# Kernel tuning notes

Measured on AMD Instinct MI355X. Metric: run time of the kernel, lower is better.

## Reference

```python
import jax, jax.numpy as jnp
import numpy as np

B, T, C, H = 2, 2048, 1024, 16
D = C // H  # head_dim = 64

def setup_inputs() -> dict:
    key = jax.random.key(0)
    k1, k2, k3 = jax.random.split(key, 3)
    x = jax.random.normal(k1, (B, T, C), dtype=jnp.float32)
    W_qkv = jax.random.normal(k2, (C, 3 * C), dtype=jnp.float32) * (C ** -0.5)
    b_qkv = jnp.zeros((3 * C,), dtype=jnp.float32)
    W_proj = jax.random.normal(k3, (C, C), dtype=jnp.float32) * (C ** -0.5)
    b_proj = jnp.zeros((C,), dtype=jnp.float32)
    return {"x": x, "W_qkv": W_qkv, "b_qkv": b_qkv, "W_proj": W_proj, "b_proj": b_proj}

def reference(x, W_qkv, b_qkv, W_proj, b_proj):
    # qkv projection: [B,T,3C]
    qkv = jnp.einsum('btc,cf->btf', x, W_qkv) + b_qkv
    q, k, v = jnp.split(qkv, 3, axis=-1)
    # split heads -> [B,H,T,D]
    q = q.reshape(B, T, H, D).transpose(0, 2, 1, 3)
    k = k.reshape(B, T, H, D).transpose(0, 2, 1, 3)
    v = v.reshape(B, T, H, D).transpose(0, 2, 1, 3)
    scale = 1.0 / jnp.sqrt(jnp.float32(D))
    att = jnp.einsum('bhqd,bhkd->bhqk', q, k) * scale  # [B,H,T,T]
    causal = jnp.tril(jnp.ones((T, T), dtype=bool))
    att = jnp.where(causal[None, None, :, :], att, jnp.float32(-jnp.inf))
    att = jax.nn.softmax(att, axis=-1)
    y = jnp.einsum('bhqk,bhkd->bhqd', att, v)  # [B,H,T,D]
    y = y.transpose(0, 2, 1, 3).reshape(B, T, C)
    return jnp.einsum('btc,cf->btf', y, W_proj) + b_proj
```

## Files before the change

### kernel.cpp

```cpp
#include <hip/hip_runtime.h>
#include <hip/hip_bf16.h>

#define Bq 2
#define Tq 2048
#define Cq 1024
#define Hq 16
#define Dq 64
#define Mq (Bq * Tq)

typedef __bf16 bf16x8 __attribute__((ext_vector_type(8)));
typedef float f32x4 __attribute__((ext_vector_type(4)));
typedef unsigned short u16;

static __device__ __forceinline__ u16 f2bf(float f) {
  union { float f; unsigned u; } v; v.f = f;
  return (u16)((v.u + 0x7fffu + ((v.u >> 16) & 1u)) >> 16);
}

static __device__ __forceinline__ f32x4 mfma16(bf16x8 a, bf16x8 b, f32x4 c) {
  return __builtin_amdgcn_mfma_f32_16x16x32_bf16(a, b, c, 0, 0, 0);
}

#define GLD16(g, l)                                                   \
  __builtin_amdgcn_global_load_lds(                                   \
      (const __attribute__((address_space(1))) unsigned int*)(g),     \
      (__attribute__((address_space(3))) unsigned int*)(l), 16, 0, 0)

static __device__ __forceinline__ int swz(int col, int row) {
  return (col & 7) + 8 * (((col >> 3) ^ (row >> 3)) & 7);
}

__global__ __launch_bounds__(256) void convert_x(const float* __restrict__ x,
                                                 u16* __restrict__ xb) {
  int i = (blockIdx.x * 256 + threadIdx.x) * 8;
  float4 a = *(const float4*)(x + i);
  float4 b = *(const float4*)(x + i + 4);
  u16 tmp[8];
  tmp[0] = f2bf(a.x); tmp[1] = f2bf(a.y); tmp[2] = f2bf(a.z); tmp[3] = f2bf(a.w);
  tmp[4] = f2bf(b.x); tmp[5] = f2bf(b.y); tmp[6] = f2bf(b.z); tmp[7] = f2bf(b.w);
  *(uint4*)(xb + i) = *(const uint4*)tmp;
}

__global__ __launch_bounds__(256) void transpose_w(const float* __restrict__ W,
                                                   u16* __restrict__ Wt,
                                                   int K, int N) {
  __shared__ __align__(16) u16 Ts[64][72];
  const int k0 = blockIdx.x * 64, n0 = blockIdx.y * 64;
  const int t = threadIdx.x;
  const int r = t >> 2, c0 = (t & 3) * 16;
  const float* src = W + (size_t)(k0 + r) * N + n0 + c0;
  u16 v16[16];
#pragma unroll
  for (int i = 0; i < 4; i++) {
    float4 f = *(const float4*)(src + 4 * i);
    v16[4 * i + 0] = f2bf(f.x); v16[4 * i + 1] = f2bf(f.y);
    v16[4 * i + 2] = f2bf(f.z); v16[4 * i + 3] = f2bf(f.w);
  }
#pragma unroll
  for (int j = 0; j < 16; j++) Ts[c0 + j][r] = v16[j];
  __syncthreads();
  u16* dst = Wt + (size_t)(n0 + r) * K + k0 + c0;
  *(uint4*)dst = *(const uint4*)&Ts[r][c0];
  *(uint4*)(dst + 8) = *(const uint4*)&Ts[r][c0 + 8];
}

__global__ __launch_bounds__(256) void qkv_gemm(
    const u16* __restrict__ A, const u16* __restrict__ Bt,
    const float* __restrict__ bias,
    u16* __restrict__ qw, u16* __restrict__ kw, u16* __restrict__ vw) {
  const int K = 1024;
  __shared__ __align__(16) u16 As[128][32];
  __shared__ __align__(16) u16 Bs[128][32];
  const int m0 = blockIdx.x * 128, n0 = blockIdx.y * 128;
  const int t = threadIdx.x, lane = t & 63, w = t >> 6;
  const int wm = (w >> 1) * 64, wn = (w & 1) * 64;
  const int l15 = lane & 15, l4 = lane >> 4;
  const int lr = lane >> 2, lc = (lane & 3) * 8;
  f32x4 acc[4][4] = {};
  const u16* ga = A + (size_t)(m0 + w * 16 + lr) * K + lc;
  const u16* gb = Bt + (size_t)(n0 + w * 16 + lr) * K + lc;

  for (int kk = 0; kk < K; kk += 32) {
    __syncthreads();
    GLD16(ga + kk, &As[w * 16][0]);
    GLD16(ga + (size_t)64 * K + kk, &As[64 + w * 16][0]);
    GLD16(gb + kk, &Bs[w * 16][0]);
    GLD16(gb + (size_t)64 * K + kk, &Bs[64 + w * 16][0]);
    __syncthreads();
    bf16x8 af[4], bfr[4];
#pragma unroll
    for (int i = 0; i < 4; i++) {
      af[i] = *(const bf16x8*)&As[wm + i * 16 + l15][l4 * 8];
      bfr[i] = *(const bf16x8*)&Bs[wn + i * 16 + l15][l4 * 8];
    }
#pragma unroll
    for (int mi = 0; mi < 4; mi++)
#pragma unroll
      for (int ni = 0; ni < 4; ni++)
        acc[mi][ni] = mfma16(af[mi], bfr[ni], acc[mi][ni]);
  }
#pragma unroll
  for (int mi = 0; mi < 4; mi++) {
#pragma unroll
    for (int ni = 0; ni < 4; ni++) {
#pragma unroll
      for (int r = 0; r < 4; r++) {
        int row = m0 + wm + mi * 16 + l4 * 4 + r;
        int col = n0 + wn + ni * 16 + l15;
        float val = acc[mi][ni][r] + bias[col];
        int which = col >> 10, c = col & 1023;
        if (which == 0) val *= 0.18033688011112042f;
        int h = c >> 6, d = c & 63;
        int b = row >> 11, tt = row & 2047;
        u16* dst = (which == 0) ? qw : ((which == 1) ? kw : vw);
        dst[(size_t)((b * Hq + h) * Tq + tt) * Dq + d] = f2bf(val);
      }
    }
  }
}

__global__ __launch_bounds__(512, 4) void attn(
    const u16* __restrict__ qw, const u16* __restrict__ kw,
    const u16* __restrict__ vw, u16* __restrict__ yw) {
  const int bh = blockIdx.x;
  const int qy = blockIdx.y;
  const int qb = (qy < 8) ? (15 - qy) : (qy - 8);
  __shared__ __align__(16) u16 Ks[64][72];
  __shared__ __align__(16) u16 Vt[64][72];
  const int t = threadIdx.x, lane = t & 63, w = t >> 6;
  const int l15 = lane & 15, l4 = lane >> 4;
  const size_t base = (size_t)bh * Tq * Dq;
  const int rv = t >> 3, c8 = t & 7;

  const int qs = qb * 128 + w * 16;
  bf16x8 qf[2];
  {
    const u16* qp = qw + base + (size_t)(qs + l15) * Dq + l4 * 8;
    qf[0] = *(const bf16x8*)qp;
    qf[1] = *(const bf16x8*)(qp + 32);
  }

  float m = -1e30f, lsum = 0.f;
  f32x4 accO[4] = {};
  const int kvmax = 2 * qb + 1;

  const u16* ksrc = kw + base + (size_t)rv * Dq + c8 * 8;
  const u16* vsrc = vw + base + (size_t)rv * Dq + c8 * 8;
  uint4 kreg = *(const uint4*)ksrc;
  uint4 vreg = *(const uint4*)vsrc;

  for (int kv = 0; kv <= kvmax; kv++) {
    __syncthreads();
    *(uint4*)&Ks[rv][c8 * 8] = kreg;
    {
      union { uint4 q; u16 s[8]; } vu; vu.q = vreg;
#pragma unroll
      for (int jj = 0; jj < 8; jj++) {
        int row = c8 * 8 + jj;
        Vt[row][swz(rv, row)] = vu.s[jj];
      }
    }
    if (kv < kvmax) {
      ksrc += 64 * Dq; vsrc += 64 * Dq;
      kreg = *(const uint4*)ksrc;
      vreg = *(const uint4*)vsrc;
    }
    __syncthreads();

    if (kv * 64 > qs + 15) continue;

    f32x4 sc[4];
    __builtin_amdgcn_s_setprio(1);
#pragma unroll
    for (int ct = 0; ct < 4; ct++) {
      bf16x8 kf0 = *(const bf16x8*)&Ks[ct * 16 + l15][l4 * 8];
      bf16x8 kf1 = *(const bf16x8*)&Ks[ct * 16 + l15][32 + l4 * 8];
      f32x4 z = {};
      z = mfma16(kf0, qf[0], z);
      z = mfma16(kf1, qf[1], z);
      sc[ct] = z;
    }
    __builtin_amdgcn_s_setprio(0);

    if (kv * 64 + 63 > qs) {
      const int q = qs + l15;
#pragma unroll
      for (int ct = 0; ct < 4; ct++)
#pragma unroll
        for (int r = 0; r < 4; r++) {
          int k = kv * 64 + ct * 16 + l4 * 4 + r;
          if (k > q) sc[ct][r] = -1e30f;
        }
    }

    float pmax = sc[0][0];
#pragma unroll
    for (int ct = 0; ct < 4; ct++)
#pragma unroll
      for (int r = 0; r < 4; r++) pmax = fmaxf(pmax, sc[ct][r]);
    pmax = fmaxf(pmax, __shfl_xor(pmax, 16));
    pmax = fmaxf(pmax, __shfl_xor(pmax, 32));

    if (__any(pmax > m + 8.f)) {
      float mn = fmaxf(m, pmax);
      float corr = exp2f(m - mn);
      m = mn;
      lsum *= corr;
#pragma unroll
      for (int r = 0; r < 4; r++) {
        float cb = __shfl(corr, (lane >> 4) * 20 + r);
#pragma unroll
        for (int dt = 0; dt < 4; dt++) accO[dt][r] *= cb;
      }
    }

    float psum = 0.f;
#pragma unroll
    for (int ct = 0; ct < 4; ct++)
#pragma unroll
      for (int r = 0; r < 4; r++) {
        float p = exp2f(sc[ct][r] - m);
        sc[ct][r] = p;
        psum += p;
      }
    psum += __shfl_xor(psum, 16);
    psum += __shfl_xor(psum, 32);
    lsum += psum;

    bf16x8 pa[2];
    const int bsrc = ((lane & 16) << 1) + l15;
#pragma unroll
    for (int h = 0; h < 2; h++) {
#pragma unroll
      for (int jh = 0; jh < 2; jh++)
#pragma unroll
        for (int r = 0; r < 4; r++) {
          float v0 = __shfl(sc[2 * h][r], bsrc + 16 * jh);
          float v1 = __shfl(sc[2 * h + 1][r], bsrc + 16 * jh);
          pa[h][jh * 4 + r] = (__bf16)((l4 & 2) ? v1 : v0);
        }
    }

    __builtin_amdgcn_s_setprio(1);
#pragma unroll
    for (int dt = 0; dt < 4; dt++) {
      int Rv = dt * 16 + l15;
      int e = (Rv >> 3) & 7;
      bf16x8 vf0 = *(const bf16x8*)&Vt[Rv][8 * ((l4 ^ e) & 7)];
      bf16x8 vf1 = *(const bf16x8*)&Vt[Rv][8 * (((4 + l4) ^ e) & 7)];
      accO[dt] = mfma16(pa[0], vf0, accO[dt]);
      accO[dt] = mfma16(pa[1], vf1, accO[dt]);
    }
    __builtin_amdgcn_s_setprio(0);
  }

  float inv = 1.0f / lsum;
  const int b = bh >> 4, hd = bh & 15;
#pragma unroll
  for (int r = 0; r < 4; r++) {
    float ib = __shfl(inv, (lane >> 4) * 20 + r);
    int tt = qs + l4 * 4 + r;
    size_t rowbase = ((size_t)(b * Tq + tt)) * Cq + hd * 64;
#pragma unroll
    for (int dt = 0; dt < 4; dt++)
      yw[rowbase + dt * 16 + l15] = f2bf(accO[dt][r] * ib);
  }
}

__global__ __launch_bounds__(256) void proj_gemm(
    const u16* __restrict__ A, const u16* __restrict__ Bt,
    const float* __restrict__ bias, float* __restrict__ out) {
  const int K = 1024, N = 1024;
  __shared__ __align__(16) u16 As[128][32];
  __shared__ __align__(16) u16 Bs[128][32];
  const int m0 = blockIdx.x * 128, n0 = blockIdx.y * 128;
  const int t = threadIdx.x, lane = t & 63, w = t >> 6;
  const int wm = (w >> 1) * 64, wn = (w & 1) * 64;
  const int l15 = lane & 15, l4 = lane >> 4;
  const int lr = lane >> 2, lc = (lane & 3) * 8;
  f32x4 acc[4][4] = {};
  const u16* ga = A + (size_t)(m0 + w * 16 + lr) * K + lc;
  const u16* gb = Bt + (size_t)(n0 + w * 16 + lr) * K + lc;

  for (int kk = 0; kk < K; kk += 32) {
    __syncthreads();
    GLD16(ga + kk, &As[w * 16][0]);
    GLD16(ga + (size_t)64 * K + kk, &As[64 + w * 16][0]);
    GLD16(gb + kk, &Bs[w * 16][0]);
    GLD16(gb + (size_t)64 * K + kk, &Bs[64 + w * 16][0]);
    __syncthreads();
    bf16x8 af[4], bfr[4];
#pragma unroll
    for (int i = 0; i < 4; i++) {
      af[i] = *(const bf16x8*)&As[wm + i * 16 + l15][l4 * 8];
      bfr[i] = *(const bf16x8*)&Bs[wn + i * 16 + l15][l4 * 8];
    }
#pragma unroll
    for (int mi = 0; mi < 4; mi++)
#pragma unroll
      for (int ni = 0; ni < 4; ni++)
        acc[mi][ni] = mfma16(af[mi], bfr[ni], acc[mi][ni]);
  }
#pragma unroll
  for (int mi = 0; mi < 4; mi++) {
#pragma unroll
    for (int ni = 0; ni < 4; ni++) {
#pragma unroll
      for (int r = 0; r < 4; r++) {
        int row = m0 + wm + mi * 16 + l4 * 4 + r;
        int col = n0 + wn + ni * 16 + l15;
        out[(size_t)row * N + col] = acc[mi][ni][r] + bias[col];
      }
    }
  }
}

extern "C" void kernel_launch(void* const* d_in, const int* in_sizes, int n_in,
                              void* d_out, int out_size, void* d_ws, size_t ws_size,
                              hipStream_t stream) {
  const float* x = (const float*)d_in[0];
  const float* W_qkv = (const float*)d_in[1];
  const float* b_qkv = (const float*)d_in[2];
  const float* W_proj = (const float*)d_in[3];
  const float* b_proj = (const float*)d_in[4];
  float* out = (float*)d_out;

  const size_t qkv_elems = (size_t)Bq * Hq * Tq * Dq;
  u16* qw = (u16*)d_ws;
  u16* kw = qw + qkv_elems;
  u16* vw = kw + qkv_elems;
  u16* xb = vw + qkv_elems;
  u16* wt = xb + (size_t)Mq * Cq;

  convert_x<<<dim3((Mq * Cq) / (256 * 8)), 256, 0, stream>>>(x, xb);
  transpose_w<<<dim3(Cq / 64, 3 * Cq / 64), 256, 0, stream>>>(W_qkv, wt, Cq, 3 * Cq);
  qkv_gemm<<<dim3(Mq / 128, 3 * Cq / 128), 256, 0, stream>>>(xb, wt, b_qkv, qw, kw, vw);
  transpose_w<<<dim3(Cq / 64, Cq / 64), 256, 0, stream>>>(W_proj, wt, Cq, Cq);
  u16* yw = xb;
  attn<<<dim3(Bq * Hq, Tq / 128), 512, 0, stream>>>(qw, kw, vw, yw);
  proj_gemm<<<dim3(Mq / 128, Cq / 128), 256, 0, stream>>>(yw, wt, b_proj, out);
}
```

Measured before the change: 207.3 us.

## Process two 16-row query tiles per wave in attention, halving block threads

The attention kernel now runs 4 waves per block instead of 8, and each wave handles 32 query rows as two 16-row sub-tiles. Each K and V fragment read from LDS therefore feeds twice as many MFMAs, and each thread stages twice as much K/V per iteration. The probability-to-bf16 conversion now uses packed v_cvt_pk_bf16_f32 and shuffles packed 32-bit words, which halves the shuffle count. In exchange, register pressure rises, causal skipping becomes coarser at 32-row granularity, and there are fewer waves per block to hide latency.

```diff
diff --git a/kernel.cpp b/kernel.cpp
--- a/kernel.cpp
+++ b/kernel.cpp
@@ -10,11 +10,18 @@
 
 typedef __bf16 bf16x8 __attribute__((ext_vector_type(8)));
 typedef float f32x4 __attribute__((ext_vector_type(4)));
+typedef unsigned uint4v __attribute__((ext_vector_type(4)));
 typedef unsigned short u16;
 
 static __device__ __forceinline__ u16 f2bf(float f) {
   union { float f; unsigned u; } v; v.f = f;
   return (u16)((v.u + 0x7fffu + ((v.u >> 16) & 1u)) >> 16);
+}
+
+static __device__ __forceinline__ unsigned cvt_pk_bf16(float a, float b) {
+  unsigned r;
+  asm("v_cvt_pk_bf16_f32 %0, %1, %2" : "=v"(r) : "v"(a), "v"(b));
+  return r;
 }
 
 static __device__ __forceinline__ f32x4 mfma16(bf16x8 a, bf16x8 b, f32x4 c) {
@@ -119,7 +126,7 @@
   }
 }
 
-__global__ __launch_bounds__(512, 4) void attn(
+__global__ __launch_bounds__(256, 3) void attn(
     const u16* __restrict__ qw, const u16* __restrict__ kw,
     const u16* __restrict__ vw, u16* __restrict__ yw) {
   const int bh = blockIdx.x;
@@ -130,115 +137,135 @@
   const int t = threadIdx.x, lane = t & 63, w = t >> 6;
   const int l15 = lane & 15, l4 = lane >> 4;
   const size_t base = (size_t)bh * Tq * Dq;
-  const int rv = t >> 3, c8 = t & 7;
-
-  const int qs = qb * 128 + w * 16;
-  bf16x8 qf[2];
+  const int rv = t >> 2, d0 = (t & 3) * 16;
+
+  const int qs0 = qb * 128 + w * 32;
+  bf16x8 qf[2][2];
   {
-    const u16* qp = qw + base + (size_t)(qs + l15) * Dq + l4 * 8;
-    qf[0] = *(const bf16x8*)qp;
-    qf[1] = *(const bf16x8*)(qp + 32);
-  }
-
-  float m = -1e30f, lsum = 0.f;
-  f32x4 accO[4] = {};
+    const u16* qp = qw + base + (size_t)(qs0 + l15) * Dq + l4 * 8;
+    qf[0][0] = *(const bf16x8*)qp;
+    qf[0][1] = *(const bf16x8*)(qp + 32);
+    qf[1][0] = *(const bf16x8*)(qp + 16 * Dq);
+    qf[1][1] = *(const bf16x8*)(qp + 16 * Dq + 32);
+  }
+
+  float m[2] = {-1e30f, -1e30f}, lsum[2] = {0.f, 0.f};
+  f32x4 accO[2][4] = {};
   const int kvmax = 2 * qb + 1;
 
-  const u16* ksrc = kw + base + (size_t)rv * Dq + c8 * 8;
-  const u16* vsrc = vw + base + (size_t)rv * Dq + c8 * 8;
-  uint4 kreg = *(const uint4*)ksrc;
-  uint4 vreg = *(const uint4*)vsrc;
+  const u16* ksrc = kw + base + (size_t)rv * Dq + d0;
+  const u16* vsrc = vw + base + (size_t)rv * Dq + d0;
+  uint4 kreg0 = *(const uint4*)ksrc, kreg1 = *(const uint4*)(ksrc + 8);
+  uint4 vreg0 = *(const uint4*)vsrc, vreg1 = *(const uint4*)(vsrc + 8);
 
   for (int kv = 0; kv <= kvmax; kv++) {
     __syncthreads();
-    *(uint4*)&Ks[rv][c8 * 8] = kreg;
+    *(uint4*)&Ks[rv][d0] = kreg0;
+    *(uint4*)&Ks[rv][d0 + 8] = kreg1;
     {
-      union { uint4 q; u16 s[8]; } vu; vu.q = vreg;
-#pragma unroll
-      for (int jj = 0; jj < 8; jj++) {
-        int row = c8 * 8 + jj;
+      union { uint4 q[2]; u16 s[16]; } vu;
+      vu.q[0] = vreg0; vu.q[1] = vreg1;
+#pragma unroll
+      for (int jj = 0; jj < 16; jj++) {
+        int row = d0 + jj;
         Vt[row][swz(rv, row)] = vu.s[jj];
       }
     }
     if (kv < kvmax) {
       ksrc += 64 * Dq; vsrc += 64 * Dq;
-      kreg = *(const uint4*)ksrc;
-      vreg = *(const uint4*)vsrc;
-    }
-    __syncthreads();
-
-    if (kv * 64 > qs + 15) continue;
-
-    f32x4 sc[4];
+      kreg0 = *(const uint4*)ksrc; kreg1 = *(const uint4*)(ksrc + 8);
+      vreg0 = *(const uint4*)vsrc; vreg1 = *(const uint4*)(vsrc + 8);
+    }
+    __syncthreads();
+
+    if (kv * 64 > qs0 + 31) continue;
+
+    f32x4 sc[2][4];
     __builtin_amdgcn_s_setprio(1);
 #pragma unroll
     for (int ct = 0; ct < 4; ct++) {
       bf16x8 kf0 = *(const bf16x8*)&Ks[ct * 16 + l15][l4 * 8];
       bf16x8 kf1 = *(const bf16x8*)&Ks[ct * 16 + l15][32 + l4 * 8];
-      f32x4 z = {};
-      z = mfma16(kf0, qf[0], z);
-      z = mfma16(kf1, qf[1], z);
-      sc[ct] = z;
+      f32x4 z0 = {};
+      z0 = mfma16(kf0, qf[0][0], z0); z0 = mfma16(kf1, qf[0][1], z0);
+      sc[0][ct] = z0;
+      f32x4 z1 = {};
+      z1 = mfma16(kf0, qf[1][0], z1); z1 = mfma16(kf1, qf[1][1], z1);
+      sc[1][ct] = z1;
     }
     __builtin_amdgcn_s_setprio(0);
 
-    if (kv * 64 + 63 > qs) {
-      const int q = qs + l15;
+    if (kv * 64 + 63 > qs0) {
+#pragma unroll
+      for (int s = 0; s < 2; s++) {
+        const int q = qs0 + s * 16 + l15;
+#pragma unroll
+        for (int ct = 0; ct < 4; ct++)
+#pragma unroll
+          for (int r = 0; r < 4; r++) {
+            int k = kv * 64 + ct * 16 + l4 * 4 + r;
+            if (k > q) sc[s][ct][r] = -1e30f;
+          }
+      }
+    }
+
+    bf16x8 pa[2][2];
+    const int bsrc = ((lane & 16) << 1) + l15;
+#pragma unroll
+    for (int s = 0; s < 2; s++) {
+      float pmax = sc[s][0][0];
 #pragma unroll
       for (int ct = 0; ct < 4; ct++)
 #pragma unroll
+        for (int r = 0; r < 4; r++) pmax = fmaxf(pmax, sc[s][ct][r]);
+      pmax = fmaxf(pmax, __shfl_xor(pmax, 16));
+      pmax = fmaxf(pmax, __shfl_xor(pmax, 32));
+
+      if (__any(pmax > m[s] + 8.f)) {
+        float mn = fmaxf(m[s], pmax);
+        float corr = exp2f(m[s] - mn);
+        m[s] = mn;
+        lsum[s] *= corr;
+#pragma unroll
         for (int r = 0; r < 4; r++) {
-          int k = kv * 64 + ct * 16 + l4 * 4 + r;
-          if (k > q) sc[ct][r] = -1e30f;
+          float cb = __shfl(corr, (lane >> 4) * 20 + r);
+#pragma unroll
+          for (int dt = 0; dt < 4; dt++) accO[s][dt][r] *= cb;
         }
-    }
-
-    float pmax = sc[0][0];
-#pragma unroll
-    for (int ct = 0; ct < 4; ct++)
-#pragma unroll
-      for (int r = 0; r < 4; r++) pmax = fmaxf(pmax, sc[ct][r]);
-    pmax = fmaxf(pmax, __shfl_xor(pmax, 16));
-    pmax = fmaxf(pmax, __shfl_xor(pmax, 32));
-
-    if (__any(pmax > m + 8.f)) {
-      float mn = fmaxf(m, pmax);
-      float corr = exp2f(m - mn);
-      m = mn;
-      lsum *= corr;
-#pragma unroll
-      for (int r = 0; r < 4; r++) {
-        float cb = __shfl(corr, (lane >> 4) * 20 + r);
-#pragma unroll
-        for (int dt = 0; dt < 4; dt++) accO[dt][r] *= cb;
-      }
-    }
-
-    float psum = 0.f;
-#pragma unroll
-    for (int ct = 0; ct < 4; ct++)
-#pragma unroll
-      for (int r = 0; r < 4; r++) {
-        float p = exp2f(sc[ct][r] - m);
-        sc[ct][r] = p;
-        psum += p;
-      }
-    psum += __shfl_xor(psum, 16);
-    psum += __shfl_xor(psum, 32);
-    lsum += psum;
-
-    bf16x8 pa[2];
-    const int bsrc = ((lane & 16) << 1) + l15;
-#pragma unroll
-    for (int h = 0; h < 2; h++) {
-#pragma unroll
-      for (int jh = 0; jh < 2; jh++)
+      }
+
+      float psum = 0.f;
+#pragma unroll
+      for (int ct = 0; ct < 4; ct++)
 #pragma unroll
         for (int r = 0; r < 4; r++) {
-          float v0 = __shfl(sc[2 * h][r], bsrc + 16 * jh);
-          float v1 = __shfl(sc[2 * h + 1][r], bsrc + 16 * jh);
-          pa[h][jh * 4 + r] = (__bf16)((l4 & 2) ? v1 : v0);
+          float p = exp2f(sc[s][ct][r] - m[s]);
+          sc[s][ct][r] = p;
+          psum += p;
         }
+      psum += __shfl_xor(psum, 16);
+      psum += __shfl_xor(psum, 32);
+      lsum[s] += psum;
+
+      unsigned pk[4][2];
+#pragma unroll
+      for (int ct = 0; ct < 4; ct++)
+#pragma unroll
+        for (int hw = 0; hw < 2; hw++)
+          pk[ct][hw] = cvt_pk_bf16(sc[s][ct][2 * hw], sc[s][ct][2 * hw + 1]);
+#pragma unroll
+      for (int h = 0; h < 2; h++) {
+        uint4v pu;
+#pragma unroll
+        for (int jh = 0; jh < 2; jh++)
+#pragma unroll
+          for (int hw = 0; hw < 2; hw++) {
+            unsigned w0 = __shfl(pk[2 * h][hw], bsrc + 16 * jh);
+            unsigned w1 = __shfl(pk[2 * h + 1][hw], bsrc + 16 * jh);
+            pu[jh * 2 + hw] = (l4 & 2) ? w1 : w0;
+          }
+        pa[s][h] = __builtin_bit_cast(bf16x8, pu);
+      }
     }
 
     __builtin_amdgcn_s_setprio(1);
@@ -248,22 +275,27 @@
       int e = (Rv >> 3) & 7;
       bf16x8 vf0 = *(const bf16x8*)&Vt[Rv][8 * ((l4 ^ e) & 7)];
       bf16x8 vf1 = *(const bf16x8*)&Vt[Rv][8 * (((4 + l4) ^ e) & 7)];
-      accO[dt] = mfma16(pa[0], vf0, accO[dt]);
-      accO[dt] = mfma16(pa[1], vf1, accO[dt]);
+      accO[0][dt] = mfma16(pa[0][0], vf0, accO[0][dt]);
+      accO[0][dt] = mfma16(pa[0][1], vf1, accO[0][dt]);
+      accO[1][dt] = mfma16(pa[1][0], vf0, accO[1][dt]);
+      accO[1][dt] = mfma16(pa[1][1], vf1, accO[1][dt]);
     }
     __builtin_amdgcn_s_setprio(0);
   }
 
-  float inv = 1.0f / lsum;
   const int b = bh >> 4, hd = bh & 15;
 #pragma unroll
-  for (int r = 0; r < 4; r++) {
-    float ib = __shfl(inv, (lane >> 4) * 20 + r);
-    int tt = qs + l4 * 4 + r;
-    size_t rowbase = ((size_t)(b * Tq + tt)) * Cq + hd * 64;
-#pragma unroll
-    for (int dt = 0; dt < 4; dt++)
-      yw[rowbase + dt * 16 + l15] = f2bf(accO[dt][r] * ib);
+  for (int s = 0; s < 2; s++) {
+    float inv = 1.0f / lsum[s];
+#pragma unroll
+    for (int r = 0; r < 4; r++) {
+      float ib = __shfl(inv, (lane >> 4) * 20 + r);
+      int tt = qs0 + s * 16 + l4 * 4 + r;
+      size_t rowbase = ((size_t)(b * Tq + tt)) * Cq + hd * 64;
+#pragma unroll
+      for (int dt = 0; dt < 4; dt++)
+        yw[rowbase + dt * 16 + l15] = f2bf(accO[s][dt][r] * ib);
+    }
   }
 }
 
@@ -337,6 +369,6 @@
   qkv_gemm<<<dim3(Mq / 128, 3 * Cq / 128), 256, 0, stream>>>(xb, wt, b_qkv, qw, kw, vw);
   transpose_w<<<dim3(Cq / 64, Cq / 64), 256, 0, stream>>>(W_proj, wt, Cq, Cq);
   u16* yw = xb;
-  attn<<<dim3(Bq * Hq, Tq / 128), 512, 0, stream>>>(qw, kw, vw, yw);
+  attn<<<dim3(Bq * Hq, Tq / 128), 256, 0, stream>>>(qw, kw, vw, yw);
   proj_gemm<<<dim3(Mq / 128, Cq / 128), 256, 0, stream>>>(yw, wt, b_proj, out);
 }
```

Measured after the change: 203.7 us. Within noise of the previous version (-1.8%).
